# Optimization experiments

Measured on AMD Instinct MI355X. Metric: run time of the kernel, lower is better.

The kernel has to match this reference:

```python
import jax, jax.numpy as jnp
import numpy as np

BLOCK = 32  # 2**basic_block

def _hadamard(n):
    H = np.array([[1.0]], dtype=np.float32)
    while H.shape[0] < n:
        H = np.block([[H, H], [H, -H]])
    return H


def setup_inputs() -> dict:
    key = jax.random.key(0)
    ks = jax.random.split(key, 9)
    B, T, I, Hd, O = 64, 512, 128, 1024, 128
    sgn = lambda k, shp: jnp.where(jax.random.normal(k, shp) >= 0, 1.0, -1.0).astype(jnp.float32)
    return {
        "x": jax.random.normal(ks[0], (B, T, I), dtype=jnp.float32),
        "W_in": jax.random.normal(ks[1], (I, Hd), dtype=jnp.float32) / np.sqrt(I),
        "s1": sgn(ks[2], (Hd,)),                      # Binadamard sign vector (layer 1)
        "b1": 0.01 * jax.random.normal(ks[3], (Hd,), dtype=jnp.float32),
        "s2": sgn(ks[4], (Hd,)),                      # Binadamard sign vector (layer 2, full)
        "b2": 0.01 * jax.random.normal(ks[5], (Hd,), dtype=jnp.float32),
        "Wbn": sgn(ks[6], (Hd, Hd)) / np.sqrt(Hd),    # BinaryNorm: sign(W)/sqrt(n), materialized
        "W_out": jax.random.normal(ks[7], (Hd, O), dtype=jnp.float32) / np.sqrt(Hd),
        "b_out": jax.random.normal(ks[8], (O,), dtype=jnp.float32),
    }


def reference(x, W_in, s1, b1, s2, b2, Wbn, W_out, b_out):
    B, T, _ = x.shape
    Hd = s1.shape[0]
    Hb = jnp.asarray(_hadamard(BLOCK) / np.sqrt(BLOCK), dtype=x.dtype)   # [32,32]
    Hf = jnp.asarray(_hadamard(Hd) / np.sqrt(Hd), dtype=x.dtype)         # [Hd,Hd]
    u = jnp.einsum('bti,ih->tbh', x, W_in)  # precompute input projections, time-major

    def step(carry, u_t):
        h1, h2 = carry
        # layer 1: block-diagonal sign*Hadamard recurrence + input
        h1 = s1 * (h1.reshape(B, -1, BLOCK) @ Hb).reshape(B, Hd) + b1 + u_t
        h1b = jax.nn.relu(h1)
        # layer 2: full sign*Hadamard recurrence + binary-norm projection of h1b
        h2 = s2 * (h2 @ Hf) + b2 + h1b @ Wbn
        return (h1, h2), None

    h0 = jnp.zeros((B, Hd), dtype=x.dtype)
    (_, h2), _ = jax.lax.scan(step, (h0, h0), u)
    h2b = jax.nn.relu(h2)
    return h2b @ W_out + b_out
```

## Files before the change

kernel.cpp:

```cpp
#include <hip/hip_runtime.h>

#define B_ 64
#define T_ 512
#define I_ 128
#define H_ 1024
#define O_ 128

typedef unsigned short u16;
typedef unsigned int u32;
typedef __attribute__((ext_vector_type(8))) short short8v;
typedef __attribute__((ext_vector_type(4))) float float4v;

typedef __attribute__((address_space(1))) const void gvoid_t;
typedef __attribute__((address_space(3))) void svoid_t;

__device__ __forceinline__ u16 f2bf(float f) {
  union { float f; u32 u; } v; v.f = f;
  u32 r = v.u + 0x7FFF + ((v.u >> 16) & 1);
  return (u16)(r >> 16);
}
__device__ __forceinline__ float bf2f(u16 b) {
  union { u32 u; float f; } v; v.u = ((u32)b) << 16;
  return v.f;
}
__device__ __forceinline__ float bits2f(u32 b) {
  union { u32 u; float f; } v; v.u = b;
  return v.f;
}

__device__ __forceinline__ float fwht32(float x, int lane) {
#pragma unroll
  for (int s = 1; s <= 16; s <<= 1) {
    const float y = __shfl_xor(x, s);
    x = (lane & s) ? (y - x) : (x + y);
  }
  return x;
}

__device__ __forceinline__ void fwht32_reg(float* x) {
#pragma unroll
  for (int s = 1; s < 32; s <<= 1)
#pragma unroll
    for (int i = 0; i < 32; ++i)
      if (!(i & s)) { const float a = x[i], b = x[i | s]; x[i] = a + b; x[i | s] = a - b; }
}

__global__ __launch_bounds__(256) void prep_xT(const float* __restrict__ x, u16* __restrict__ xT) {
  int idx = blockIdx.x * 256 + threadIdx.x;
  int i = idx & (I_ - 1);
  int r = idx >> 7;
  int b = r & (B_ - 1);
  int t = r >> 6;
  xT[idx] = f2bf(x[((size_t)b * T_ + t) * I_ + i]);
}

__global__ __launch_bounds__(256) void transpose_bf16(const float* __restrict__ in, u16* __restrict__ out,
                                                      int K, int N) {
  int idx = blockIdx.x * 256 + threadIdx.x;
  if (idx >= K * N) return;
  int n = idx / K, k = idx - n * K;
  out[idx] = f2bf(in[(size_t)k * N + n]);
}

template <int K, bool BIAS>
__global__ __launch_bounds__(256) void gemm_bf16(const u16* __restrict__ A, const u16* __restrict__ Bt,
                                                 u16* __restrict__ C, const float* __restrict__ bias) {
  __shared__ u16 As[128 * 64];
  __shared__ u16 Bs[128 * 64];
  const int tid = threadIdx.x;
  const int bm = blockIdx.x, bn = blockIdx.y;
  const int lane = tid & 63, w = tid >> 6;
  const int wr = w >> 1, wc = w & 1;
  const int l16 = lane & 15, lq = lane >> 4;

  float4v acc[4][4];
#pragma unroll
  for (int mi = 0; mi < 4; ++mi)
#pragma unroll
    for (int ni = 0; ni < 4; ++ni)
#pragma unroll
      for (int j = 0; j < 4; ++j) acc[mi][ni][j] = 0.f;

  const int srow = w * 32 + (lane >> 3);
  const int scol = (((lane & 7) ^ (lane >> 3)) << 3);
  const u16* Ag = A + (size_t)(bm * 128 + srow) * K + scol;
  const u16* Bg = Bt + (size_t)(bn * 128 + srow) * K + scol;

  for (int k0 = 0; k0 < K; k0 += 64) {
    __syncthreads();
#pragma unroll
    for (int i = 0; i < 4; ++i) {
      __builtin_amdgcn_global_load_lds((gvoid_t*)(Ag + k0 + (size_t)i * 8 * K),
                                       (svoid_t*)&As[(w * 32 + i * 8) * 64], 16, 0, 0);
      __builtin_amdgcn_global_load_lds((gvoid_t*)(Bg + k0 + (size_t)i * 8 * K),
                                       (svoid_t*)&Bs[(w * 32 + i * 8) * 64], 16, 0, 0);
    }
    __syncthreads();
#pragma unroll
    for (int ks = 0; ks < 2; ++ks) {
      short8v a[4], bf[4];
#pragma unroll
      for (int mi = 0; mi < 4; ++mi) {
        const int row = wr * 64 + mi * 16 + l16;
        a[mi] = *(const short8v*)&As[row * 64 + (((ks * 4 + lq) ^ (row & 7)) << 3)];
      }
#pragma unroll
      for (int ni = 0; ni < 4; ++ni) {
        const int row = wc * 64 + ni * 16 + l16;
        bf[ni] = *(const short8v*)&Bs[row * 64 + (((ks * 4 + lq) ^ (row & 7)) << 3)];
      }
#pragma unroll
      for (int mi = 0; mi < 4; ++mi)
#pragma unroll
        for (int ni = 0; ni < 4; ++ni)
          acc[mi][ni] = __builtin_amdgcn_mfma_f32_16x16x32_bf16(a[mi], bf[ni], acc[mi][ni], 0, 0, 0);
    }
  }

#pragma unroll
  for (int mi = 0; mi < 4; ++mi)
#pragma unroll
    for (int ni = 0; ni < 4; ++ni) {
      const int row = bm * 128 + wr * 64 + mi * 16 + lq * 4;
      const int col = bn * 128 + wc * 64 + ni * 16 + l16;
      const float bv = BIAS ? bias[col] : 0.f;
#pragma unroll
      for (int j = 0; j < 4; ++j) C[(size_t)(row + j) * H_ + col] = f2bf(acc[mi][ni][j] + bv);
    }
}

__global__ __launch_bounds__(1024) void h1_Pinit(const float* __restrict__ s1, float* __restrict__ P) {
  const int hb = blockIdx.x;
  const int tid = threadIdx.x;
  const int j = tid >> 5, r = tid & 31;
  const int lane = tid & 63;
  const float sc = s1[hb * 32 + r] * 0.17677669529663687f;
  float x = (r == j) ? 1.f : 0.f;
  for (int it = 0; it < 32; ++it) x = sc * fwht32(x, lane);
  P[(size_t)hb * 1024 + r * 32 + j] = x;
}

__global__ __launch_bounds__(64) void h1_local(const u16* __restrict__ u, const float* __restrict__ s1,
                                               float* __restrict__ Ybuf) {
  const int g = blockIdx.x * 64 + threadIdx.x;
  const int hb = g & 31, b = (g >> 5) & 63, chunk = g >> 11;
  float x[32], sc[32];
#pragma unroll
  for (int i = 0; i < 32; i += 4) {
    const float4 s4 = *(const float4*)&s1[hb * 32 + i];
    sc[i] = s4.x * 0.17677669529663687f;
    sc[i + 1] = s4.y * 0.17677669529663687f;
    sc[i + 2] = s4.z * 0.17677669529663687f;
    sc[i + 3] = s4.w * 0.17677669529663687f;
  }
#pragma unroll
  for (int i = 0; i < 32; ++i) x[i] = 0.f;
  const u16* up = u + ((size_t)(chunk * 32) * B_ + b) * H_ + hb * 32;
#pragma unroll 2
  for (int k = 0; k < 32; ++k) {
    u32 wv[16];
#pragma unroll
    for (int j = 0; j < 4; ++j) {
      const uint4 t4 = *(const uint4*)(up + (size_t)k * (B_ * H_) + j * 8);
      wv[4 * j] = t4.x; wv[4 * j + 1] = t4.y; wv[4 * j + 2] = t4.z; wv[4 * j + 3] = t4.w;
    }
    fwht32_reg(x);
#pragma unroll
    for (int i2 = 0; i2 < 16; ++i2) {
      x[2 * i2]     = fmaf(sc[2 * i2],     x[2 * i2],     bits2f(wv[i2] << 16));
      x[2 * i2 + 1] = fmaf(sc[2 * i2 + 1], x[2 * i2 + 1], bits2f(wv[i2] & 0xFFFF0000u));
    }
  }
  float* yp = Ybuf + (size_t)g * 32;
#pragma unroll
  for (int i = 0; i < 32; i += 4) {
    float4 o; o.x = x[i]; o.y = x[i + 1]; o.z = x[i + 2]; o.w = x[i + 3];
    *(float4*)(yp + i) = o;
  }
}

__global__ __launch_bounds__(64) void h1_carry(const float* __restrict__ P, const float* __restrict__ Ybuf,
                                               float* __restrict__ Zbuf) {
  const int hpair = blockIdx.x, b = blockIdx.y;
  const int lane = threadIdx.x;
  const int r = lane & 31, hb = hpair * 2 + (lane >> 5);
  const float* Prow = P + (size_t)hb * 1024 + r * 32;
  float pr[32];
#pragma unroll
  for (int j = 0; j < 32; ++j) pr[j] = Prow[j];
  float z = 0.f;
  const int base = lane & 32;
  for (int c = 0; c < 16; ++c) {
    Zbuf[(((size_t)c * 64 + b) * 32 + hb) * 32 + r] = z;
    if (c < 15) {
      const float yv = Ybuf[(((size_t)c * 64 + b) * 32 + hb) * 32 + r];
      float zn = 0.f;
#pragma unroll
      for (int j = 0; j < 32; ++j) zn = fmaf(pr[j], __shfl(z, base + j), zn);
      z = zn + yv;
    }
  }
}

__global__ __launch_bounds__(64) void h1_apply(u16* __restrict__ u, const float* __restrict__ s1,
                                               const float* __restrict__ Zbuf) {
  const int g = blockIdx.x * 64 + threadIdx.x;
  const int hb = g & 31, b = (g >> 5) & 63, chunk = g >> 11;
  float x[32], sc[32];
#pragma unroll
  for (int i = 0; i < 32; i += 4) {
    const float4 s4 = *(const float4*)&s1[hb * 32 + i];
    sc[i] = s4.x * 0.17677669529663687f;
    sc[i + 1] = s4.y * 0.17677669529663687f;
    sc[i + 2] = s4.z * 0.17677669529663687f;
    sc[i + 3] = s4.w * 0.17677669529663687f;
  }
  const float* zp = Zbuf + (size_t)g * 32;
#pragma unroll
  for (int i = 0; i < 32; i += 4) {
    const float4 z4 = *(const float4*)(zp + i);
    x[i] = z4.x; x[i + 1] = z4.y; x[i + 2] = z4.z; x[i + 3] = z4.w;
  }
  u16* up = u + ((size_t)(chunk * 32) * B_ + b) * H_ + hb * 32;
#pragma unroll 2
  for (int k = 0; k < 32; ++k) {
    u32 wv[16];
#pragma unroll
    for (int j = 0; j < 4; ++j) {
      const uint4 t4 = *(const uint4*)(up + (size_t)k * (B_ * H_) + j * 8);
      wv[4 * j] = t4.x; wv[4 * j + 1] = t4.y; wv[4 * j + 2] = t4.z; wv[4 * j + 3] = t4.w;
    }
    fwht32_reg(x);
#pragma unroll
    for (int i2 = 0; i2 < 16; ++i2) {
      x[2 * i2]     = fmaf(sc[2 * i2],     x[2 * i2],     bits2f(wv[i2] << 16));
      x[2 * i2 + 1] = fmaf(sc[2 * i2 + 1], x[2 * i2 + 1], bits2f(wv[i2] & 0xFFFF0000u));
    }
    u32 ov[16];
#pragma unroll
    for (int i2 = 0; i2 < 16; ++i2) {
      const u32 lo = f2bf(fmaxf(x[2 * i2], 0.f));
      const u32 hi = f2bf(fmaxf(x[2 * i2 + 1], 0.f));
      ov[i2] = lo | (hi << 16);
    }
#pragma unroll
    for (int j = 0; j < 4; ++j) {
      uint4 t4; t4.x = ov[4 * j]; t4.y = ov[4 * j + 1]; t4.z = ov[4 * j + 2]; t4.w = ov[4 * j + 3];
      *(uint4*)(up + (size_t)k * (B_ * H_) + j * 8) = t4;
    }
  }
}

__device__ __forceinline__ void fwht1024(float* x, int lane) {
#pragma unroll
  for (int s = 1; s < 16; s <<= 1)
#pragma unroll
    for (int r = 0; r < 16; ++r)
      if (!(r & s)) { float a0 = x[r], b0 = x[r | s]; x[r] = a0 + b0; x[r | s] = a0 - b0; }
#pragma unroll
  for (int s = 0; s < 6; ++s) {
    const int m = 1 << s;
    const bool hi = (lane & m) != 0;
#pragma unroll
    for (int r = 0; r < 16; ++r) {
      const float y = __shfl_xor(x[r], m);
      x[r] = hi ? (y - x[r]) : (x[r] + y);
    }
  }
}

__global__ __launch_bounds__(256) void fwht_chunk(const u16* __restrict__ V, const float* __restrict__ s2,
                                                  u16* __restrict__ A32, u16* __restrict__ Y) {
  const int W = blockIdx.x * 4 + (threadIdx.x >> 6);
  const int lane = threadIdx.x & 63;
  float x[16], sc[16];
  if (W < 1024) {
#pragma unroll
    for (int r = 0; r < 16; ++r) {
      const int idx = r * 64 + lane;
      sc[r] = s2[idx] * 0.03125f;
      x[r] = (idx == W) ? 1.f : 0.f;
    }
    for (int it = 0; it < 32; ++it) {
#pragma unroll
      for (int r = 0; r < 16; ++r) x[r] *= sc[r];
      fwht1024(x, lane);
    }
    u16* dst = A32 + (size_t)W * H_ + lane;
#pragma unroll
    for (int r = 0; r < 16; ++r) dst[r * 64] = f2bf(x[r]);
  } else {
    const int W2 = W - 1024;
    const int c = W2 >> 6, b = W2 & 63;
#pragma unroll
    for (int r = 0; r < 16; ++r) { sc[r] = s2[r * 64 + lane] * 0.03125f; x[r] = 0.f; }
    const u16* p = V + ((size_t)(c * 32) * B_ + b) * H_ + lane;
    const size_t stride = (size_t)B_ * H_;
    u16 v[16];
#pragma unroll
    for (int r = 0; r < 16; ++r) v[r] = p[r * 64];
    for (int j = 0; j < 32; ++j) {
      u16 vn[16];
      if (j + 1 < 32) {
        const u16* pn = p + (size_t)(j + 1) * stride;
#pragma unroll
        for (int r = 0; r < 16; ++r) vn[r] = pn[r * 64];
      }
      fwht1024(x, lane);
#pragma unroll
      for (int r = 0; r < 16; ++r) x[r] = sc[r] * x[r] + bf2f(v[r]);
      if (j + 1 < 32) {
#pragma unroll
        for (int r = 0; r < 16; ++r) v[r] = vn[r];
      }
    }
    u16* dst = Y + ((size_t)c * B_ + b) * H_ + lane;
#pragma unroll
    for (int r = 0; r < 16; ++r) dst[r * 64] = f2bf(x[r]);
  }
}

template <bool FIRST, bool LAST>
__global__ __launch_bounds__(256) void combine(const u16* __restrict__ Zold, const u16* __restrict__ Yc,
                                               const u16* __restrict__ A32, u16* __restrict__ Znew,
                                               float* __restrict__ h2out) {
  const int rt = blockIdx.x >> 6, nt = blockIdx.x & 63;
  const int tid = threadIdx.x;
  __shared__ float red[4][16][16];
  if (!FIRST) {
    const int w = tid >> 6, lane = tid & 63, l16 = lane & 15, lq = lane >> 4;
    float4v acc = {0.f, 0.f, 0.f, 0.f};
    const u16* Ap = Zold + (size_t)(rt * 16 + l16) * H_ + w * 256 + lq * 8;
    const u16* Bp = A32 + (size_t)(nt * 16 + l16) * H_ + w * 256 + lq * 8;
#pragma unroll
    for (int ks = 0; ks < 8; ++ks) {
      short8v a = *(const short8v*)(Ap + ks * 32);
      short8v bb = *(const short8v*)(Bp + ks * 32);
      acc = __builtin_amdgcn_mfma_f32_16x16x32_bf16(a, bb, acc, 0, 0, 0);
    }
#pragma unroll
    for (int j = 0; j < 4; ++j) red[w][lq * 4 + j][l16] = acc[j];
    __syncthreads();
  } else {
    __syncthreads();
  }
  const int row = tid >> 4, col = tid & 15;
  float s = 0.f;
  if (!FIRST) s = red[0][row][col] + red[1][row][col] + red[2][row][col] + red[3][row][col];
  const int b = rt * 16 + row, n = nt * 16 + col;
  s += bf2f(Yc[(size_t)b * H_ + n]);
  if (LAST) h2out[(size_t)b * H_ + n] = s;
  else Znew[(size_t)b * H_ + n] = f2bf(s);
}

__global__ __launch_bounds__(128) void final_out(const float* __restrict__ h2, const float* __restrict__ W_out,
                                                 const float* __restrict__ b_out, float* __restrict__ out) {
  __shared__ float hrow[H_];
  const int b = blockIdx.x, o = threadIdx.x;
  for (int i = o; i < H_; i += 128) hrow[i] = fmaxf(h2[(size_t)b * H_ + i], 0.f);
  __syncthreads();
  float acc = b_out[o];
  for (int h = 0; h < H_; ++h) acc = fmaf(hrow[h], W_out[(size_t)h * O_ + o], acc);
  out[b * O_ + o] = acc;
}

extern "C" void kernel_launch(void* const* d_in, const int* in_sizes, int n_in,
                              void* d_out, int out_size, void* d_ws, size_t ws_size,
                              hipStream_t stream) {
  const float* x     = (const float*)d_in[0];
  const float* W_in  = (const float*)d_in[1];
  const float* s1    = (const float*)d_in[2];
  const float* b1    = (const float*)d_in[3];
  const float* s2    = (const float*)d_in[4];
  const float* b2    = (const float*)d_in[5];
  const float* Wbn   = (const float*)d_in[6];
  const float* W_out = (const float*)d_in[7];
  const float* b_out = (const float*)d_in[8];
  float* out = (float*)d_out;

  char* ws = (char*)d_ws;
  u16* u      = (u16*)ws;
  u16* V      = (u16*)(ws + 67108864);
  float* P1   = (float*)(ws + 67108864);
  u16* xT     = (u16*)(ws + 134217728);
  float* Ybuf = (float*)(ws + 134217728);
  float* Zbuf = (float*)(ws + 138412032);
  u16* WbnT   = (u16*)(ws + 142606336);
  u16* WinT   = (u16*)(ws + 144703488);
  u16* A32    = (u16*)(ws + 134217728);
  u16* Y      = (u16*)(ws + 136314880);
  u16* Zb0    = (u16*)(ws + 138412032);
  u16* Zb1    = (u16*)(ws + 138543104);
  float* h2   = (float*)(ws + 138674176);

  prep_xT<<<16384, 256, 0, stream>>>(x, xT);
  transpose_bf16<<<4096, 256, 0, stream>>>(Wbn, WbnT, 1024, 1024);
  transpose_bf16<<<512, 256, 0, stream>>>(W_in, WinT, 128, 1024);
  h1_Pinit<<<32, 1024, 0, stream>>>(s1, P1);
  gemm_bf16<128, true><<<dim3(256, 8), 256, 0, stream>>>(xT, WinT, u, b1);
  h1_local<<<512, 64, 0, stream>>>(u, s1, Ybuf);
  h1_carry<<<dim3(16, 64), 64, 0, stream>>>(P1, Ybuf, Zbuf);
  h1_apply<<<512, 64, 0, stream>>>(u, s1, Zbuf);
  gemm_bf16<1024, true><<<dim3(256, 8), 256, 0, stream>>>(u, WbnT, V, b2);
  fwht_chunk<<<512, 256, 0, stream>>>(V, s2, A32, Y);

  u16* Zb[2] = {Zb0, Zb1};
  combine<true, false><<<256, 256, 0, stream>>>(nullptr, Y, A32, Zb[0], nullptr);
  for (int c = 1; c < 15; ++c)
    combine<false, false><<<256, 256, 0, stream>>>(Zb[(c + 1) & 1], Y + (size_t)c * B_ * H_, A32,
                                                   Zb[c & 1], nullptr);
  combine<false, true><<<256, 256, 0, stream>>>(Zb[0], Y + (size_t)15 * B_ * H_, A32, nullptr, h2);

  final_out<<<64, 128, 0, stream>>>(h2, W_out, b_out, out);
}
```

Baseline: 353.5 us.

## Rebalance chunked scans: shorter layer-1 chunks, longer layer-2 chunks via squared transition

Layer-1 chunk length drops from 32 to 16 steps, doubling parallel local/apply work and lengthening the serial carry to 32 chunks. Layer-2 chunks grow from 32 to 64 steps, and the 64-step transition matrix is built by squaring the 32-step one with a new GEMM. This halves the number of serial combine launches from 16 to 8. The GEMM grid axes are also swapped for a different block order. The cost is a longer layer-1 carry chain, longer fwht_chunk sweeps, one extra GEMM, and more workspace.

```diff
diff --git a/kernel.cpp b/kernel.cpp
--- a/kernel.cpp
+++ b/kernel.cpp
@@ -68,7 +68,7 @@
   __shared__ u16 As[128 * 64];
   __shared__ u16 Bs[128 * 64];
   const int tid = threadIdx.x;
-  const int bm = blockIdx.x, bn = blockIdx.y;
+  const int bn = blockIdx.x, bm = blockIdx.y;
   const int lane = tid & 63, w = tid >> 6;
   const int wr = w >> 1, wc = w & 1;
   const int l16 = lane & 15, lq = lane >> 4;
@@ -126,6 +126,70 @@
       const float bv = BIAS ? bias[col] : 0.f;
 #pragma unroll
       for (int j = 0; j < 4; ++j) C[(size_t)(row + j) * H_ + col] = f2bf(acc[mi][ni][j] + bv);
+    }
+}
+
+__global__ __launch_bounds__(256) void gemm_sq(const u16* __restrict__ A, u16* __restrict__ C) {
+  __shared__ u16 As[128][40];
+  __shared__ u16 Bs[128][40];
+  const int tid = threadIdx.x;
+  const int bn = blockIdx.x, bm = blockIdx.y;
+  const int lane = tid & 63, w = tid >> 6;
+  const int wr = w >> 1, wc = w & 1;
+  const int l16 = lane & 15, lq = lane >> 4;
+
+  float4v acc[4][4];
+#pragma unroll
+  for (int mi = 0; mi < 4; ++mi)
+#pragma unroll
+    for (int ni = 0; ni < 4; ++ni)
+#pragma unroll
+      for (int j = 0; j < 4; ++j) acc[mi][ni][j] = 0.f;
+
+  const int sr = tid >> 1;
+  const int sc = (tid & 1) << 4;
+  const u16* Ag = A + (size_t)(bm * 128 + sr) * 1024 + sc;
+  const int kr = tid >> 4;
+  const int no = (tid & 15) * 8;
+
+  for (int k0 = 0; k0 < 1024; k0 += 32) {
+    uint4 a0 = *(const uint4*)(Ag + k0);
+    uint4 a1 = *(const uint4*)(Ag + k0 + 8);
+    uint4 b0 = *(const uint4*)(A + (size_t)(k0 + kr) * 1024 + bn * 128 + no);
+    uint4 b1 = *(const uint4*)(A + (size_t)(k0 + 16 + kr) * 1024 + bn * 128 + no);
+    __syncthreads();
+    *(uint4*)&As[sr][sc] = a0;
+    *(uint4*)&As[sr][sc + 8] = a1;
+    {
+      u16 tmp[8];
+      *(uint4*)tmp = b0;
+#pragma unroll
+      for (int i = 0; i < 8; ++i) Bs[no + i][kr] = tmp[i];
+      *(uint4*)tmp = b1;
+#pragma unroll
+      for (int i = 0; i < 8; ++i) Bs[no + i][16 + kr] = tmp[i];
+    }
+    __syncthreads();
+    short8v a[4], bf[4];
+#pragma unroll
+    for (int mi = 0; mi < 4; ++mi) a[mi] = *(const short8v*)&As[wr * 64 + mi * 16 + l16][lq * 8];
+#pragma unroll
+    for (int ni = 0; ni < 4; ++ni) bf[ni] = *(const short8v*)&Bs[wc * 64 + ni * 16 + l16][lq * 8];
+#pragma unroll
+    for (int mi = 0; mi < 4; ++mi)
+#pragma unroll
+      for (int ni = 0; ni < 4; ++ni)
+        acc[mi][ni] = __builtin_amdgcn_mfma_f32_16x16x32_bf16(a[mi], bf[ni], acc[mi][ni], 0, 0, 0);
+  }
+
+#pragma unroll
+  for (int mi = 0; mi < 4; ++mi)
+#pragma unroll
+    for (int ni = 0; ni < 4; ++ni) {
+      const int row = bm * 128 + wr * 64 + mi * 16 + lq * 4;
+      const int col = bn * 128 + wc * 64 + ni * 16 + l16;
+#pragma unroll
+      for (int j = 0; j < 4; ++j) C[(size_t)(row + j) * H_ + col] = f2bf(acc[mi][ni][j]);
     }
 }
 
@@ -136,7 +200,7 @@
   const int lane = tid & 63;
   const float sc = s1[hb * 32 + r] * 0.17677669529663687f;
   float x = (r == j) ? 1.f : 0.f;
-  for (int it = 0; it < 32; ++it) x = sc * fwht32(x, lane);
+  for (int it = 0; it < 16; ++it) x = sc * fwht32(x, lane);
   P[(size_t)hb * 1024 + r * 32 + j] = x;
 }
 
@@ -155,9 +219,9 @@
   }
 #pragma unroll
   for (int i = 0; i < 32; ++i) x[i] = 0.f;
-  const u16* up = u + ((size_t)(chunk * 32) * B_ + b) * H_ + hb * 32;
+  const u16* up = u + ((size_t)(chunk * 16) * B_ + b) * H_ + hb * 32;
 #pragma unroll 2
-  for (int k = 0; k < 32; ++k) {
+  for (int k = 0; k < 16; ++k) {
     u32 wv[16];
 #pragma unroll
     for (int j = 0; j < 4; ++j) {
@@ -190,9 +254,9 @@
   for (int j = 0; j < 32; ++j) pr[j] = Prow[j];
   float z = 0.f;
   const int base = lane & 32;
-  for (int c = 0; c < 16; ++c) {
+  for (int c = 0; c < 32; ++c) {
     Zbuf[(((size_t)c * 64 + b) * 32 + hb) * 32 + r] = z;
-    if (c < 15) {
+    if (c < 31) {
       const float yv = Ybuf[(((size_t)c * 64 + b) * 32 + hb) * 32 + r];
       float zn = 0.f;
 #pragma unroll
@@ -221,9 +285,9 @@
     const float4 z4 = *(const float4*)(zp + i);
     x[i] = z4.x; x[i + 1] = z4.y; x[i + 2] = z4.z; x[i + 3] = z4.w;
   }
-  u16* up = u + ((size_t)(chunk * 32) * B_ + b) * H_ + hb * 32;
+  u16* up = u + ((size_t)(chunk * 16) * B_ + b) * H_ + hb * 32;
 #pragma unroll 2
-  for (int k = 0; k < 32; ++k) {
+  for (int k = 0; k < 16; ++k) {
     u32 wv[16];
 #pragma unroll
     for (int j = 0; j < 4; ++j) {
@@ -294,14 +358,14 @@
     const int c = W2 >> 6, b = W2 & 63;
 #pragma unroll
     for (int r = 0; r < 16; ++r) { sc[r] = s2[r * 64 + lane] * 0.03125f; x[r] = 0.f; }
-    const u16* p = V + ((size_t)(c * 32) * B_ + b) * H_ + lane;
+    const u16* p = V + ((size_t)(c * 64) * B_ + b) * H_ + lane;
     const size_t stride = (size_t)B_ * H_;
     u16 v[16];
 #pragma unroll
     for (int r = 0; r < 16; ++r) v[r] = p[r * 64];
-    for (int j = 0; j < 32; ++j) {
+    for (int j = 0; j < 64; ++j) {
       u16 vn[16];
-      if (j + 1 < 32) {
+      if (j + 1 < 64) {
         const u16* pn = p + (size_t)(j + 1) * stride;
 #pragma unroll
         for (int r = 0; r < 16; ++r) vn[r] = pn[r * 64];
@@ -309,7 +373,7 @@
       fwht1024(x, lane);
 #pragma unroll
       for (int r = 0; r < 16; ++r) x[r] = sc[r] * x[r] + bf2f(v[r]);
-      if (j + 1 < 32) {
+      if (j + 1 < 64) {
 #pragma unroll
         for (int r = 0; r < 16; ++r) v[r] = vn[r];
       }
@@ -322,7 +386,7 @@
 
 template <bool FIRST, bool LAST>
 __global__ __launch_bounds__(256) void combine(const u16* __restrict__ Zold, const u16* __restrict__ Yc,
-                                               const u16* __restrict__ A32, u16* __restrict__ Znew,
+                                               const u16* __restrict__ A64, u16* __restrict__ Znew,
                                                float* __restrict__ h2out) {
   const int rt = blockIdx.x >> 6, nt = blockIdx.x & 63;
   const int tid = threadIdx.x;
@@ -331,7 +395,7 @@
     const int w = tid >> 6, lane = tid & 63, l16 = lane & 15, lq = lane >> 4;
     float4v acc = {0.f, 0.f, 0.f, 0.f};
     const u16* Ap = Zold + (size_t)(rt * 16 + l16) * H_ + w * 256 + lq * 8;
-    const u16* Bp = A32 + (size_t)(nt * 16 + l16) * H_ + w * 256 + lq * 8;
+    const u16* Bp = A64 + (size_t)(nt * 16 + l16) * H_ + w * 256 + lq * 8;
 #pragma unroll
     for (int ks = 0; ks < 8; ++ks) {
       short8v a = *(const short8v*)(Ap + ks * 32);
@@ -382,34 +446,36 @@
   u16* u      = (u16*)ws;
   u16* V      = (u16*)(ws + 67108864);
   float* P1   = (float*)(ws + 67108864);
+  float* Zbuf = (float*)(ws + 69206016);
   u16* xT     = (u16*)(ws + 134217728);
   float* Ybuf = (float*)(ws + 134217728);
-  float* Zbuf = (float*)(ws + 138412032);
   u16* WbnT   = (u16*)(ws + 142606336);
   u16* WinT   = (u16*)(ws + 144703488);
   u16* A32    = (u16*)(ws + 134217728);
   u16* Y      = (u16*)(ws + 136314880);
-  u16* Zb0    = (u16*)(ws + 138412032);
-  u16* Zb1    = (u16*)(ws + 138543104);
-  float* h2   = (float*)(ws + 138674176);
+  u16* A64    = (u16*)(ws + 137363456);
+  u16* Zb0    = (u16*)(ws + 139460608);
+  u16* Zb1    = (u16*)(ws + 139591680);
+  float* h2   = (float*)(ws + 139722752);
 
   prep_xT<<<16384, 256, 0, stream>>>(x, xT);
   transpose_bf16<<<4096, 256, 0, stream>>>(Wbn, WbnT, 1024, 1024);
   transpose_bf16<<<512, 256, 0, stream>>>(W_in, WinT, 128, 1024);
   h1_Pinit<<<32, 1024, 0, stream>>>(s1, P1);
-  gemm_bf16<128, true><<<dim3(256, 8), 256, 0, stream>>>(xT, WinT, u, b1);
-  h1_local<<<512, 64, 0, stream>>>(u, s1, Ybuf);
+  gemm_bf16<128, true><<<dim3(8, 256), 256, 0, stream>>>(xT, WinT, u, b1);
+  h1_local<<<1024, 64, 0, stream>>>(u, s1, Ybuf);
   h1_carry<<<dim3(16, 64), 64, 0, stream>>>(P1, Ybuf, Zbuf);
-  h1_apply<<<512, 64, 0, stream>>>(u, s1, Zbuf);
-  gemm_bf16<1024, true><<<dim3(256, 8), 256, 0, stream>>>(u, WbnT, V, b2);
-  fwht_chunk<<<512, 256, 0, stream>>>(V, s2, A32, Y);
+  h1_apply<<<1024, 64, 0, stream>>>(u, s1, Zbuf);
+  gemm_bf16<1024, true><<<dim3(8, 256), 256, 0, stream>>>(u, WbnT, V, b2);
+  fwht_chunk<<<384, 256, 0, stream>>>(V, s2, A32, Y);
+  gemm_sq<<<dim3(8, 8), 256, 0, stream>>>(A32, A64);
 
   u16* Zb[2] = {Zb0, Zb1};
-  combine<true, false><<<256, 256, 0, stream>>>(nullptr, Y, A32, Zb[0], nullptr);
-  for (int c = 1; c < 15; ++c)
-    combine<false, false><<<256, 256, 0, stream>>>(Zb[(c + 1) & 1], Y + (size_t)c * B_ * H_, A32,
+  combine<true, false><<<256, 256, 0, stream>>>(nullptr, Y, A64, Zb[0], nullptr);
+  for (int c = 1; c < 7; ++c)
+    combine<false, false><<<256, 256, 0, stream>>>(Zb[(c + 1) & 1], Y + (size_t)c * B_ * H_, A64,
                                                    Zb[c & 1], nullptr);
-  combine<false, true><<<256, 256, 0, stream>>>(Zb[0], Y + (size_t)15 * B_ * H_, A32, nullptr, h2);
+  combine<false, true><<<256, 256, 0, stream>>>(Zb[0], Y + (size_t)7 * B_ * H_, A64, nullptr, h2);
 
   final_out<<<64, 128, 0, stream>>>(h2, W_out, b_out, out);
 }
```

Measured after the change: 442.1 us. 1.25x slower.
